# Performance work log

Measured on AMD Instinct MI355X. Metric: run time of the kernel, lower is better.

The kernel has to match this reference:

```python
import jax, jax.numpy as jnp
import numpy as np

B, S, E, H = 4, 2048, 1024, 16
D = E // H

def setup_inputs() -> dict:
    key = jax.random.key(0)
    ks = jax.random.split(key, 8)
    sc = lambda fan_in: 1.0 / np.sqrt(fan_in)
    return {
        "query": jax.random.normal(ks[0], (B, S, E), jnp.float32),
        "Wq": jax.random.normal(ks[1], (E, E), jnp.float32) * sc(E),
        "bq": jnp.zeros((E,), jnp.float32),
        "Wk": jax.random.normal(ks[2], (E, E), jnp.float32) * sc(E),
        "bk": jnp.zeros((E,), jnp.float32),
        "Wv": jax.random.normal(ks[3], (E, E), jnp.float32) * sc(E),
        "bv": jnp.zeros((E,), jnp.float32),
        "Wo": jax.random.normal(ks[4], (E, E), jnp.float32) * sc(E),
        "bo": jnp.zeros((E,), jnp.float32),
        "Wm1": jax.random.normal(ks[5], (E // 4, E), jnp.float32) * sc(E),
        "bm1": jnp.zeros((E // 4,), jnp.float32),
        "Wm2": jax.random.normal(ks[6], (E, E // 4), jnp.float32) * sc(E // 4),
        "bm2": jnp.zeros((E,), jnp.float32),
        "dopamine": jnp.ones((1,), jnp.float32),
        "serotonin": jnp.ones((1,), jnp.float32),
        "norepinephrine": jnp.ones((1,), jnp.float32),
        "acetylcholine": jnp.ones((1,), jnp.float32),
        "attn_scale": jnp.ones((1,), jnp.float32),
        "attn_bias": jnp.zeros((1,), jnp.float32),
    }

def reference(query, Wq, bq, Wk, bk, Wv, bv, Wo, bo,
              Wm1, bm1, Wm2, bm2,
              dopamine, serotonin, norepinephrine, acetylcholine,
              attn_scale, attn_bias):
    scale = D ** (-0.5)
    # projections (nn.Linear: y = x @ W.T + b)
    q = (query @ Wq.T + bq).reshape(B, S, H, D).transpose(0, 2, 1, 3)  # [B,H,S,D]
    k = (query @ Wk.T + bk).reshape(B, S, H, D).transpose(0, 2, 1, 3)
    v = (query @ Wv.T + bv).reshape(B, S, H, D).transpose(0, 2, 1, 3)
    scores = jnp.einsum('bhqd,bhkd->bhqk', q, k) * scale  # [B,H,S,S]
    probs = jax.nn.softmax(scores, axis=-1)
    attn = jnp.einsum('bhqk,bhkd->bhqd', probs, v)  # [B,H,S,D]
    # neuromodulation: MLP on query, summed scalar-weighted effects / 4
    mod = jax.nn.relu(query @ Wm1.T + bm1) @ Wm2.T + bm2  # [B,S,E]
    nm_gain = (dopamine + serotonin + norepinephrine + acetylcholine) / 4.0  # [1]
    neuromod = (mod * nm_gain).reshape(B, S, H, D).transpose(0, 2, 1, 3)  # [B,H,S,D]
    attn = (attn * attn_scale + attn_bias) * (1.0 + neuromod)
    attn = attn.transpose(0, 2, 1, 3).reshape(B, S, E)
    return attn @ Wo.T + bo
```

## Files before the change

kernel.cpp:

```cpp
#include <hip/hip_runtime.h>
#include <hip/hip_bf16.h>
#include <cstdint>

#define PB 4
#define PS 2048
#define PE 1024
#define PH 16
#define PD 64
#define PM (PB * PS)

typedef __attribute__((ext_vector_type(8))) _Float16 half8;
typedef __attribute__((ext_vector_type(4))) float f32x4;

#define MFMAH __builtin_amdgcn_mfma_f32_16x16x32_f16

#define GLOAD_LDS(gp, lp) __builtin_amdgcn_global_load_lds(                    \
    (const __attribute__((address_space(1))) void*)(gp),                       \
    (__attribute__((address_space(3))) void*)(lp), 16, 0, 0)

#if __has_builtin(__builtin_amdgcn_exp2f)
#define FAST_EXP2 1
#else
#define FAST_EXP2 0
#endif

__device__ inline unsigned short h16(float x) {
    _Float16 h = (_Float16)x;
    unsigned short u;
    __builtin_memcpy(&u, &h, 2);
    return u;
}
__device__ inline unsigned pkrtz(float a, float b) {
    auto p = __builtin_amdgcn_cvt_pkrtz(a, b);
    unsigned u;
    __builtin_memcpy(&u, &p, 4);
    return u;
}

__global__ __launch_bounds__(256)
void split_all(const float* __restrict__ q,   const float* __restrict__ wq,
               const float* __restrict__ wk,  const float* __restrict__ wv,
               const float* __restrict__ wo,  const float* __restrict__ wm1,
               const float* __restrict__ wm2,
               unsigned short* qh,  unsigned short* wqh, unsigned short* wkh,
               unsigned short* wvh, unsigned short* woh,
               unsigned short* m1h, unsigned short* m2h)
{
    const int b = blockIdx.x;
    const float* src; unsigned short* dst; int base;
    if      (b <  8192) { src = q;   dst = qh;  base = 0;     }
    else if (b <  9216) { src = wq;  dst = wqh; base = 8192;  }
    else if (b < 10240) { src = wk;  dst = wkh; base = 9216;  }
    else if (b < 11264) { src = wv;  dst = wvh; base = 10240; }
    else if (b < 12288) { src = wo;  dst = woh; base = 11264; }
    else if (b < 12544) { src = wm1; dst = m1h; base = 12288; }
    else                { src = wm2; dst = m2h; base = 12544; }
    const int i = (b - base) * 256 + threadIdx.x;
    float4 f = ((const float4*)src)[i];
    ushort4 h;
    h.x = h16(f.x); h.y = h16(f.y); h.z = h16(f.z); h.w = h16(f.w);
    ((ushort4*)dst)[i] = h;
}

template<int MODE, bool RELU>
__global__ __launch_bounds__(256, 2)
void gemm_pl(const unsigned short* __restrict__ Ah,
             const unsigned short* __restrict__ Bh,
             const float* __restrict__ bias, float* __restrict__ C,
             unsigned short* __restrict__ Oh,
             int M, int N, int K,
             const float* __restrict__ attn,
             const float* __restrict__ g0, const float* __restrict__ g1,
             const float* __restrict__ g2, const float* __restrict__ g3,
             const float* __restrict__ asc, const float* __restrict__ abi)
{
    __shared__ int4 ldsq[4096];
    char* const lds = (char*)ldsq;

    const int tid  = threadIdx.x;
    const int lane = tid & 63;
    const int w    = tid >> 6;
    const int lq   = lane & 15;
    const int lg   = lane >> 4;
    const int wm   = (w >> 1) * 64;
    const int wn   = (w & 1) * 64;
    const int m0   = blockIdx.x * 128;
    const int n0   = blockIdx.y * 128;

    const unsigned short* const gp =
        (w < 2) ? Ah + (size_t)m0 * K : Bh + (size_t)n0 * K;
    const int pb    = (w < 2) ? 0 : 16384;
    const int ch0   = (w & 1) * 8;
    const int scol8 = (((lane & 7) ^ (lane >> 3)) << 3);
    const int lrow8 = lane >> 3;

    auto ISSUE = [&](int k0, int bufn) {
        #pragma unroll
        for (int r = 0; r < 8; ++r) {
            const int c   = ch0 + r;
            const int row = c * 8 + lrow8;
            GLOAD_LDS(gp + (size_t)row * K + k0 + scol8,
                      lds + bufn * 32768 + pb + c * 1024 + 16 * lane);
        }
    };

    f32x4 acc[4][4];
    #pragma unroll
    for (int mt = 0; mt < 4; ++mt)
        #pragma unroll
        for (int nt = 0; nt < 4; ++nt)
            acc[mt][nt] = (f32x4){0.f, 0.f, 0.f, 0.f};

    ISSUE(0, 0);
    __syncthreads();

    int buf = 0;
    for (int k0 = 0; k0 < K; k0 += 64) {
        if (k0 + 64 < K) ISSUE(k0 + 64, buf ^ 1);

        const char* const L = lds + buf * 32768;
        #pragma unroll
        for (int kh = 0; kh < 2; ++kh) {
            half8 af[4];
            #pragma unroll
            for (int mt = 0; mt < 4; ++mt) {
                const int row = wm + 16 * mt + lq;
                const int off = row * 128 + ((kh * 64 + 16 * lg) ^ ((row & 7) << 4));
                af[mt] = *(const half8*)(L + off);
            }
            #pragma unroll
            for (int nt = 0; nt < 4; ++nt) {
                const int row = wn + 16 * nt + lq;
                const int off = row * 128 + ((kh * 64 + 16 * lg) ^ ((row & 7) << 4));
                half8 bf = *(const half8*)(L + 16384 + off);
                #pragma unroll
                for (int mt = 0; mt < 4; ++mt)
                    acc[mt][nt] = MFMAH(af[mt], bf, acc[mt][nt], 0, 0, 0);
            }
        }
        __syncthreads();
        buf ^= 1;
    }

    float gain = 0.f, ascv = 0.f, abiv = 0.f;
    if (MODE == 6) {
        gain = 0.25f * (*g0 + *g1 + *g2 + *g3);
        ascv = *asc;
        abiv = *abi;
    }

    #pragma unroll
    for (int nt = 0; nt < 4; ++nt) {
        const int n  = n0 + wn + 16 * nt + lq;
        const float bv = bias[n];
        #pragma unroll
        for (int mt = 0; mt < 4; ++mt) {
            #pragma unroll
            for (int j = 0; j < 4; ++j) {
                const int m = m0 + wm + 16 * mt + 4 * lg + j;
                float v = acc[mt][nt][j] + bv;
                if (RELU) v = fmaxf(v, 0.f);
                if (MODE == 0) {
                    C[(size_t)m * N + n] = v;
                } else if (MODE == 1) {
                    const int b = m >> 11, s = m & 2047;
                    const int h = n >> 6, d = n & 63;
                    C[((size_t)(b * PH + h) * PS + s) * PD + d] = v;
                } else if (MODE == 3) {
                    const int b = m >> 11, s = m & 2047;
                    const int h = n >> 6, d = n & 63;
                    Oh[((size_t)(b * PH + h) * PS + s) * PD + d] = h16(v);
                } else if (MODE == 4) {
                    const int b = m >> 11;
                    const int h = n >> 6, d = n & 63;
                    const int scol = (m & 2047 & ~63) + ((mt & 1) << 5)
                                   + (lg << 3) + ((mt >> 1) << 2) + j;
                    Oh[((size_t)(b * PH + h) * PD + d) * PS + scol] = h16(v);
                } else if (MODE == 5) {
                    Oh[(size_t)m * N + n] = h16(v);
                } else {
                    const int b = m >> 11, s = m & 2047;
                    const int h = n >> 6, d = n & 63;
                    const float av = attn[((size_t)(b * PH + h) * PS + s) * PD + d];
                    const float o = (av * ascv + abiv) * (1.f + v * gain);
                    Oh[(size_t)m * N + n] = h16(o);
                }
            }
        }
    }
}

typedef __attribute__((ext_vector_type(8))) short short8;
#define MFMA16 __builtin_amdgcn_mfma_f32_16x16x32_bf16
__device__ inline unsigned short bf16rn(float x) {
    unsigned u = __builtin_bit_cast(unsigned, x);
    u += 0x7FFFu + ((u >> 16) & 1u);
    return (unsigned short)(u >> 16);
}
__device__ inline float bf16tof(unsigned short h) {
    unsigned u = ((unsigned)h) << 16;
    return __builtin_bit_cast(float, u);
}
__device__ inline void split2(float x, unsigned short& h, unsigned short& l) {
    h = bf16rn(x);
    l = bf16rn(x - bf16tof(h));
}

template<int MODE, bool RELU>
__global__ __launch_bounds__(256, 2)
void gemm_nt(const float* __restrict__ A, const float* __restrict__ Bw,
             const float* __restrict__ bias, float* __restrict__ C,
             unsigned short* __restrict__ Ohi,
             int M, int N, int K,
             const float* __restrict__ attn,
             const float* __restrict__ g0, const float* __restrict__ g1,
             const float* __restrict__ g2, const float* __restrict__ g3,
             const float* __restrict__ asc, const float* __restrict__ abi)
{
    __shared__ int4 ldsq[4096];
    char* const lds = (char*)ldsq;

    const int tid  = threadIdx.x;
    const int lane = tid & 63;
    const int w    = tid >> 6;
    const int lq   = lane & 15;
    const int lg   = lane >> 4;
    const int wm   = (w >> 1) * 64;
    const int wn   = (w & 1) * 64;
    const int m0   = blockIdx.x * 128;
    const int n0   = blockIdx.y * 128;

    const int irow = tid >> 3;
    const int ic8  = (tid & 7) * 8;
    const int woff = (ic8 * 2);

    f32x4 acc[4][4];
    #pragma unroll
    for (int mt = 0; mt < 4; ++mt)
        #pragma unroll
        for (int nt = 0; nt < 4; ++nt)
            acc[mt][nt] = (f32x4){0.f, 0.f, 0.f, 0.f};

    for (int k0 = 0; k0 < K; k0 += 64) {
        #pragma unroll
        for (int mat = 0; mat < 2; ++mat) {
            const float* const src = mat ? Bw : A;
            const int rbase = mat ? n0 : m0;
            const int pbase = mat ? 32768 : 0;
            #pragma unroll
            for (int r = 0; r < 4; ++r) {
                const int row = irow + 32 * r;
                const float* p = src + (size_t)(rbase + row) * K + k0 + ic8;
                float4 f0 = *(const float4*)p;
                float4 f1 = *(const float4*)(p + 4);
                short8 vh, vl;
                {
                    unsigned short h, l;
                    split2(f0.x, h, l); vh[0] = (short)h; vl[0] = (short)l;
                    split2(f0.y, h, l); vh[1] = (short)h; vl[1] = (short)l;
                    split2(f0.z, h, l); vh[2] = (short)h; vl[2] = (short)l;
                    split2(f0.w, h, l); vh[3] = (short)h; vl[3] = (short)l;
                    split2(f1.x, h, l); vh[4] = (short)h; vl[4] = (short)l;
                    split2(f1.y, h, l); vh[5] = (short)h; vl[5] = (short)l;
                    split2(f1.z, h, l); vh[6] = (short)h; vl[6] = (short)l;
                    split2(f1.w, h, l); vh[7] = (short)h; vl[7] = (short)l;
                }
                const int off = row * 128 + (woff ^ ((row & 7) << 4));
                *(short8*)(lds + pbase + off)         = vh;
                *(short8*)(lds + pbase + 16384 + off) = vl;
            }
        }
        __syncthreads();

        #pragma unroll
        for (int kh = 0; kh < 2; ++kh) {
            short8 afh[4], afl[4];
            #pragma unroll
            for (int mt = 0; mt < 4; ++mt) {
                const int row = wm + 16 * mt + lq;
                const int off = row * 128 + ((kh * 64 + 16 * lg) ^ ((row & 7) << 4));
                afh[mt] = *(const short8*)(lds + off);
                afl[mt] = *(const short8*)(lds + 16384 + off);
            }
            #pragma unroll
            for (int nt = 0; nt < 4; ++nt) {
                const int row = wn + 16 * nt + lq;
                const int off = row * 128 + ((kh * 64 + 16 * lg) ^ ((row & 7) << 4));
                short8 bfh = *(const short8*)(lds + 32768 + off);
                short8 bfl = *(const short8*)(lds + 49152 + off);
                #pragma unroll
                for (int mt = 0; mt < 4; ++mt) {
                    acc[mt][nt] = MFMA16(afh[mt], bfh, acc[mt][nt], 0, 0, 0);
                    acc[mt][nt] = MFMA16(afh[mt], bfl, acc[mt][nt], 0, 0, 0);
                    acc[mt][nt] = MFMA16(afl[mt], bfh, acc[mt][nt], 0, 0, 0);
                }
            }
        }
        __syncthreads();
    }

    float gain = 0.f, ascv = 0.f, abiv = 0.f;
    if (MODE == 2) {
        gain = 0.25f * (*g0 + *g1 + *g2 + *g3);
        ascv = *asc;
        abiv = *abi;
    }

    #pragma unroll
    for (int nt = 0; nt < 4; ++nt) {
        const int n  = n0 + wn + 16 * nt + lq;
        const float bv = bias[n];
        #pragma unroll
        for (int mt = 0; mt < 4; ++mt) {
            #pragma unroll
            for (int j = 0; j < 4; ++j) {
                const int m = m0 + wm + 16 * mt + 4 * lg + j;
                float v = acc[mt][nt][j] + bv;
                if (RELU) v = fmaxf(v, 0.f);
                if (MODE == 0) {
                    C[(size_t)m * N + n] = v;
                } else if (MODE == 1) {
                    const int b = m >> 11, s = m & 2047;
                    const int h = n >> 6, d = n & 63;
                    C[((size_t)(b * PH + h) * PS + s) * PD + d] = v;
                } else if (MODE == 3) {
                    const int b = m >> 11, s = m & 2047;
                    const int h = n >> 6, d = n & 63;
                    Ohi[((size_t)(b * PH + h) * PS + s) * PD + d] = h16(v);
                } else if (MODE == 4) {
                    const int b = m >> 11;
                    const int h = n >> 6, d = n & 63;
                    const int scol = (m & 2047 & ~63) + ((mt & 1) << 5)
                                   + (lg << 3) + ((mt >> 1) << 2) + j;
                    Ohi[((size_t)(b * PH + h) * PD + d) * PS + scol] = h16(v);
                } else {
                    const int b = m >> 11, s = m & 2047;
                    const int h = n >> 6, d = n & 63;
                    const float av = attn[((size_t)(b * PH + h) * PS + s) * PD + d];
                    C[(size_t)m * N + n] = (av * ascv + abiv) * (1.f + v * gain);
                }
            }
        }
    }
}

__global__ __launch_bounds__(256, 2)
void flash_mfma(const float* qf,
                const unsigned short* __restrict__ kf,
                const unsigned short* __restrict__ vtf,
                float* attn)
{
    __shared__ int4 ldsv[2048];
    char* const ldsb = (char*)ldsv;

    const int tid  = threadIdx.x;
    const int lane = tid & 63;
    const int w    = tid >> 6;
    const int lq   = lane & 15;
    const int lg   = lane >> 4;

    const int L  = blockIdx.x + (blockIdx.y << 4) + (blockIdx.z << 8);
    const int nL = ((L & 7) << 7) + (L >> 3);
    const int bh = nL >> 4;
    const int q0 = (nL & 15) * 128 + w * 32;

    const size_t kbase = (size_t)bh * PS * PD;
    const size_t vbase = (size_t)bh * PD * PS;

    const unsigned short* const gp = (w < 2) ? kf + kbase : vtf + vbase;
    const bool isK = (w < 2);
    const int ch0   = (w & 1) * 4;
    const int scol8 = (((lane & 7) ^ (lane >> 3)) << 3);
    const int lrow8 = lane >> 3;

    auto ISSUE = [&](int kt, int bufn) {
        #pragma unroll
        for (int r = 0; r < 4; ++r) {
            const int c   = ch0 + r;
            const int row = c * 8 + lrow8;
            const size_t goff = isK ? (size_t)(kt + row) * PD + scol8
                                    : (size_t)row * PS + kt + scol8;
            GLOAD_LDS(gp + goff,
                      ldsb + bufn * 16384 + (isK ? 0 : 8192) + c * 1024 + 16 * lane);
        }
    };

    const half8 onesh = {(_Float16)1.f, (_Float16)1.f, (_Float16)1.f,
                         (_Float16)1.f, (_Float16)1.f, (_Float16)1.f,
                         (_Float16)1.f, (_Float16)1.f};

#if FAST_EXP2
    const float QSCALE = 0.125f * 1.4426950408889634f;
    const float THR    = 11.5415603f;
#define EXP_P(x) __builtin_amdgcn_exp2f(x)
#else
    const float QSCALE = 0.125f;
    const float THR    = 8.f;
#define EXP_P(x) __expf(x)
#endif

    half8 qh[2][2];
    #pragma unroll
    for (int u = 0; u < 2; ++u) {
        const float* qp = qf + ((size_t)bh * PS + q0 + 16 * u + lq) * PD + 8 * lg;
        #pragma unroll
        for (int t = 0; t < 2; ++t)
            #pragma unroll
            for (int b = 0; b < 8; ++b)
                qh[u][t][b] = (_Float16)(qp[t * 32 + b] * QSCALE);
    }

    f32x4 ot[2][4];
    #pragma unroll
    for (int u = 0; u < 2; ++u)
        #pragma unroll
        for (int mt = 0; mt < 4; ++mt)
            ot[u][mt] = (f32x4){0.f, 0.f, 0.f, 0.f};
    f32x4 lacc[2] = {{0.f,0.f,0.f,0.f}, {0.f,0.f,0.f,0.f}};
    float m_run[2] = {-3.0e38f, -3.0e38f};

    ISSUE(0, 0);
    __syncthreads();

    int buf = 0;
    for (int kti = 0; kti < PS / 64; ++kti) {
        const bool pf = (kti + 1 < PS / 64);
        if (pf) ISSUE((kti + 1) * 64, buf ^ 1);

        const char* const L2 = ldsb + buf * 16384;

        f32x4 st[2][4];
        #pragma unroll
        for (int mt = 0; mt < 4; ++mt) {
            const int row = 16 * mt + lq;
            const int swz = (row & 7) << 4;
            const char* kr = L2 + row * 128;
            half8 a0 = *(const half8*)(kr + ((16 * lg) ^ swz));
            half8 a1 = *(const half8*)(kr + ((64 + 16 * lg) ^ swz));
            #pragma unroll
            for (int u = 0; u < 2; ++u) {
                f32x4 acc = {0.f, 0.f, 0.f, 0.f};
                acc = MFMAH(a0, qh[u][0], acc, 0, 0, 0);
                acc = MFMAH(a1, qh[u][1], acc, 0, 0, 0);
                st[u][mt] = acc;
            }
        }

        half8 pb[2][2];
        #pragma unroll
        for (int u = 0; u < 2; ++u) {
            float a0 = fmaxf(fmaxf(st[u][0][0], st[u][0][1]), st[u][0][2]);
            float a1 = fmaxf(fmaxf(st[u][0][3], st[u][1][0]), st[u][1][1]);
            float a2 = fmaxf(fmaxf(st[u][1][2], st[u][1][3]), st[u][2][0]);
            float a3 = fmaxf(fmaxf(st[u][2][1], st[u][2][2]), st[u][2][3]);
            float a4 = fmaxf(fmaxf(st[u][3][0], st[u][3][1]), st[u][3][2]);
            float b0 = fmaxf(fmaxf(a0, a1), a2);
            float b1 = fmaxf(fmaxf(a3, a4), st[u][3][3]);
            float pmax = fmaxf(b0, b1);
            pmax = fmaxf(pmax, __shfl_xor(pmax, 16));
            pmax = fmaxf(pmax, __shfl_xor(pmax, 32));
            if (!__all(pmax - m_run[u] <= THR)) {
                float mnew = fmaxf(m_run[u], pmax);
                float corr = EXP_P(m_run[u] - mnew);
                m_run[u] = mnew;
                #pragma unroll
                for (int j = 0; j < 4; ++j)
                    lacc[u][j] *= corr;
                #pragma unroll
                for (int mt = 0; mt < 4; ++mt)
                    #pragma unroll
                    for (int j = 0; j < 4; ++j)
                        ot[u][mt][j] *= corr;
            }
            #pragma unroll
            for (int mt = 0; mt < 4; ++mt)
                #pragma unroll
                for (int j = 0; j < 4; ++j)
                    st[u][mt][j] = EXP_P(st[u][mt][j] - m_run[u]);
            #pragma unroll
            for (int t = 0; t < 2; ++t) {
                unsigned w0 = pkrtz(st[u][t][0],     st[u][t][1]);
                unsigned w1 = pkrtz(st[u][t][2],     st[u][t][3]);
                unsigned w2 = pkrtz(st[u][t + 2][0], st[u][t + 2][1]);
                unsigned w3 = pkrtz(st[u][t + 2][2], st[u][t + 2][3]);
                uint4 pw = make_uint4(w0, w1, w2, w3);
                __builtin_memcpy(&pb[u][t], &pw, 16);
            }
            lacc[u] = MFMAH(onesh, pb[u][0], lacc[u], 0, 0, 0);
            lacc[u] = MFMAH(onesh, pb[u][1], lacc[u], 0, 0, 0);
        }

        #pragma unroll
        for (int t = 0; t < 2; ++t) {
            #pragma unroll
            for (int mt = 0; mt < 4; ++mt) {
                const int row = 16 * mt + lq;
                const int swz = (row & 7) << 4;
                const char* vr = L2 + 8192 + row * 128;
                half8 vv = *(const half8*)(vr + ((t * 64 + 16 * lg) ^ swz));
                #pragma unroll
                for (int u = 0; u < 2; ++u)
                    ot[u][mt] = MFMAH(vv, pb[u][t], ot[u][mt], 0, 0, 0);
            }
        }

        __syncthreads();
        buf ^= 1;
    }

    #pragma unroll
    for (int u = 0; u < 2; ++u) {
        const float inv = 1.f / lacc[u][0];
        float* op = attn + ((size_t)bh * PS + q0 + 16 * u + lq) * PD + 4 * lg;
        #pragma unroll
        for (int mt = 0; mt < 4; ++mt) {
            float4 o;
            o.x = ot[u][mt][0] * inv; o.y = ot[u][mt][1] * inv;
            o.z = ot[u][mt][2] * inv; o.w = ot[u][mt][3] * inv;
            *(float4*)(op + 16 * mt) = o;
        }
    }
}

extern "C" void kernel_launch(void* const* d_in, const int* in_sizes, int n_in,
                              void* d_out, int out_size, void* d_ws, size_t ws_size,
                              hipStream_t stream)
{
    const float* query = (const float*)d_in[0];
    const float* Wq  = (const float*)d_in[1];  const float* bq  = (const float*)d_in[2];
    const float* Wk  = (const float*)d_in[3];  const float* bk  = (const float*)d_in[4];
    const float* Wv  = (const float*)d_in[5];  const float* bv  = (const float*)d_in[6];
    const float* Wo  = (const float*)d_in[7];  const float* bo  = (const float*)d_in[8];
    const float* Wm1 = (const float*)d_in[9];  const float* bm1 = (const float*)d_in[10];
    const float* Wm2 = (const float*)d_in[11]; const float* bm2 = (const float*)d_in[12];
    const float* dop = (const float*)d_in[13];
    const float* ser = (const float*)d_in[14];
    const float* nor = (const float*)d_in[15];
    const float* ach = (const float*)d_in[16];
    const float* asc = (const float*)d_in[17];
    const float* abi = (const float*)d_in[18];
    float* out = (float*)d_out;

    char* wsb = (char*)d_ws;
    float*          qf32 = (float*)wsb;
    unsigned short* kf   = (unsigned short*)(wsb + (32u << 20));
    unsigned short* vtf  = (unsigned short*)(wsb + (48u << 20));

    dim3 blk(256);
    const bool presplit = (ws_size >= 161480704ull);

    if (presplit) {
        unsigned short* h1h   = (unsigned short*)(wsb + (64u << 20));
        unsigned short* afh   = (unsigned short*)(wsb + (72u << 20));
        unsigned short* qh    = (unsigned short*)(wsb + (104u << 20));
        unsigned short* wqh   = (unsigned short*)(wsb + (136u << 20));
        unsigned short* wkh   = (unsigned short*)(wsb + (138u << 20));
        unsigned short* wvh   = (unsigned short*)(wsb + (140u << 20));
        unsigned short* woh   = (unsigned short*)(wsb + (142u << 20));
        unsigned short* m1h   = (unsigned short*)(wsb + (144u << 20));
        unsigned short* m2h   = (unsigned short*)(wsb + (145u << 20));

        split_all<<<12800, blk, 0, stream>>>(
            query, Wq, Wk, Wv, Wo, Wm1, Wm2,
            qh, wqh, wkh, wvh, woh, m1h, m2h);

        gemm_pl<1, false><<<dim3(PM / 128, PE / 128), blk, 0, stream>>>(
            qh, wqh, bq, qf32, nullptr, PM, PE, PE,
            nullptr, nullptr, nullptr, nullptr, nullptr, nullptr, nullptr);
        gemm_pl<3, false><<<dim3(PM / 128, PE / 128), blk, 0, stream>>>(
            qh, wkh, bk, nullptr, kf, PM, PE, PE,
            nullptr, nullptr, nullptr, nullptr, nullptr, nullptr, nullptr);
        gemm_pl<4, false><<<dim3(PM / 128, PE / 128), blk, 0, stream>>>(
            qh, wvh, bv, nullptr, vtf, PM, PE, PE,
            nullptr, nullptr, nullptr, nullptr, nullptr, nullptr, nullptr);
        gemm_pl<5, true><<<dim3(PM / 128, 256 / 128), blk, 0, stream>>>(
            qh, m1h, bm1, nullptr, h1h, PM, 256, PE,
            nullptr, nullptr, nullptr, nullptr, nullptr, nullptr, nullptr);

        flash_mfma<<<dim3(PS / 128, PH, PB), blk, 0, stream>>>(
            qf32, kf, vtf, qf32);

        gemm_pl<6, false><<<dim3(PM / 128, PE / 128), blk, 0, stream>>>(
            h1h, m2h, bm2, nullptr, afh, PM, PE, 256,
            qf32, dop, ser, nor, ach, asc, abi);
        gemm_pl<0, false><<<dim3(PM / 128, PE / 128), blk, 0, stream>>>(
            afh, woh, bo, out, nullptr, PM, PE, PE,
            nullptr, nullptr, nullptr, nullptr, nullptr, nullptr, nullptr);
    } else {
        float* h1    = (float*)(wsb + (64u << 20));
        float* attnf = (float*)(wsb + (72u << 20));

        gemm_nt<1, false><<<dim3(PM / 128, PE / 128), blk, 0, stream>>>(
            query, Wq, bq, qf32, nullptr, PM, PE, PE,
            nullptr, nullptr, nullptr, nullptr, nullptr, nullptr, nullptr);
        gemm_nt<3, false><<<dim3(PM / 128, PE / 128), blk, 0, stream>>>(
            query, Wk, bk, nullptr, kf, PM, PE, PE,
            nullptr, nullptr, nullptr, nullptr, nullptr, nullptr, nullptr);
        gemm_nt<4, false><<<dim3(PM / 128, PE / 128), blk, 0, stream>>>(
            query, Wv, bv, nullptr, vtf, PM, PE, PE,
            nullptr, nullptr, nullptr, nullptr, nullptr, nullptr, nullptr);
        gemm_nt<0, true><<<dim3(PM / 128, 256 / 128), blk, 0, stream>>>(
            query, Wm1, bm1, h1, nullptr, PM, 256, PE,
            nullptr, nullptr, nullptr, nullptr, nullptr, nullptr, nullptr);

        flash_mfma<<<dim3(PS / 128, PH, PB), blk, 0, stream>>>(
            qf32, kf, vtf, qf32);

        gemm_nt<2, false><<<dim3(PM / 128, PE / 128), blk, 0, stream>>>(
            h1, Wm2, bm2, attnf, nullptr, PM, PE, 256,
            qf32, dop, ser, nor, ach, asc, abi);
        gemm_nt<0, false><<<dim3(PM / 128, PE / 128), blk, 0, stream>>>(
            attnf, Wo, bo, out, nullptr, PM, PE, PE,
            nullptr, nullptr, nullptr, nullptr, nullptr, nullptr, nullptr);
    }
}
```

Measured before the change: 228.4 us.

## Fuse Q, K, V projections into one GEMM kernel sharing the A tile

Replaces three separate projection GEMM launches with a single 512-thread kernel that loads one 128-row activation tile and three 128-column weight tiles per K step. Each block computes Q, K and V outputs together, so the shared input tile is read from global memory once instead of three times and two launches go away. The cost is 128 KB of double-buffered LDS per block and a larger accumulator footprint per thread, which can limit occupancy.

```diff
diff --git a/kernel.cpp b/kernel.cpp
--- a/kernel.cpp
+++ b/kernel.cpp
@@ -62,6 +62,118 @@
     ((ushort4*)dst)[i] = h;
 }
 
+__global__ __launch_bounds__(512, 2)
+void gemm_qkv(const unsigned short* __restrict__ Ah,
+              const unsigned short* __restrict__ Wqh,
+              const unsigned short* __restrict__ Wkh,
+              const unsigned short* __restrict__ Wvh,
+              const float* __restrict__ bq, const float* __restrict__ bk,
+              const float* __restrict__ bv,
+              float* __restrict__ qf32, unsigned short* __restrict__ kf,
+              unsigned short* __restrict__ vtf)
+{
+    __shared__ int4 ldsq[8192];
+    char* const lds = (char*)ldsq;
+    const int K = PE;
+
+    const int tid  = threadIdx.x;
+    const int lane = tid & 63;
+    const int w    = tid >> 6;
+    const int lq   = lane & 15;
+    const int lg   = lane >> 4;
+    const int wr   = w >> 2;
+    const int wc   = w & 3;
+    const int m0   = blockIdx.x * 128;
+    const int n0   = blockIdx.y * 128;
+
+    const int plane = w >> 1;
+    const unsigned short* const gp =
+        (plane == 0) ? Ah  + (size_t)m0 * K :
+        (plane == 1) ? Wqh + (size_t)n0 * K :
+        (plane == 2) ? Wkh + (size_t)n0 * K :
+                       Wvh + (size_t)n0 * K;
+    const int pbase = plane * 16384;
+    const int ch0   = (w & 1) * 8;
+    const int scol8 = (((lane & 7) ^ (lane >> 3)) << 3);
+    const int lrow8 = lane >> 3;
+
+    auto ISSUE = [&](int k0, int bufn) {
+        #pragma unroll
+        for (int r = 0; r < 8; ++r) {
+            const int c   = ch0 + r;
+            const int row = c * 8 + lrow8;
+            GLOAD_LDS(gp + (size_t)row * K + k0 + scol8,
+                      lds + bufn * 65536 + pbase + c * 1024 + 16 * lane);
+        }
+    };
+
+    f32x4 acc[3][4][2];
+    #pragma unroll
+    for (int o = 0; o < 3; ++o)
+        #pragma unroll
+        for (int mt = 0; mt < 4; ++mt)
+            #pragma unroll
+            for (int nt = 0; nt < 2; ++nt)
+                acc[o][mt][nt] = (f32x4){0.f, 0.f, 0.f, 0.f};
+
+    ISSUE(0, 0);
+    __syncthreads();
+
+    int buf = 0;
+    for (int k0 = 0; k0 < K; k0 += 64) {
+        if (k0 + 64 < K) ISSUE(k0 + 64, buf ^ 1);
+
+        const char* const L = lds + buf * 65536;
+        #pragma unroll
+        for (int kh = 0; kh < 2; ++kh) {
+            half8 af[4];
+            #pragma unroll
+            for (int mt = 0; mt < 4; ++mt) {
+                const int row = 64 * wr + 16 * mt + lq;
+                const int off = row * 128 + ((kh * 64 + 16 * lg) ^ ((row & 7) << 4));
+                af[mt] = *(const half8*)(L + off);
+            }
+            #pragma unroll
+            for (int o = 0; o < 3; ++o) {
+                #pragma unroll
+                for (int nt = 0; nt < 2; ++nt) {
+                    const int row = 32 * wc + 16 * nt + lq;
+                    const int off = row * 128 + ((kh * 64 + 16 * lg) ^ ((row & 7) << 4));
+                    half8 bf = *(const half8*)(L + 16384 * (o + 1) + off);
+                    #pragma unroll
+                    for (int mt = 0; mt < 4; ++mt)
+                        acc[o][mt][nt] = MFMAH(af[mt], bf, acc[o][mt][nt], 0, 0, 0);
+                }
+            }
+        }
+        __syncthreads();
+        buf ^= 1;
+    }
+
+    #pragma unroll
+    for (int nt = 0; nt < 2; ++nt) {
+        const int n = n0 + 32 * wc + 16 * nt + lq;
+        const int h = n >> 6, d = n & 63;
+        const float bqv = bq[n], bkv = bk[n], bvv = bv[n];
+        #pragma unroll
+        for (int mt = 0; mt < 4; ++mt) {
+            #pragma unroll
+            for (int j = 0; j < 4; ++j) {
+                const int m = m0 + 64 * wr + 16 * mt + 4 * lg + j;
+                const int b = m >> 11, s = m & 2047;
+                qf32[((size_t)(b * PH + h) * PS + s) * PD + d] =
+                    acc[0][mt][nt][j] + bqv;
+                kf[((size_t)(b * PH + h) * PS + s) * PD + d] =
+                    h16(acc[1][mt][nt][j] + bkv);
+                const int scol = (s & ~63) + ((mt & 1) << 5) + (lg << 3)
+                               + ((mt >> 1) << 2) + j;
+                vtf[((size_t)(b * PH + h) * PD + d) * PS + scol] =
+                    h16(acc[2][mt][nt][j] + bvv);
+            }
+        }
+    }
+}
+
 template<int MODE, bool RELU>
 __global__ __launch_bounds__(256, 2)
 void gemm_pl(const unsigned short* __restrict__ Ah,
@@ -162,20 +274,6 @@
                 if (RELU) v = fmaxf(v, 0.f);
                 if (MODE == 0) {
                     C[(size_t)m * N + n] = v;
-                } else if (MODE == 1) {
-                    const int b = m >> 11, s = m & 2047;
-                    const int h = n >> 6, d = n & 63;
-                    C[((size_t)(b * PH + h) * PS + s) * PD + d] = v;
-                } else if (MODE == 3) {
-                    const int b = m >> 11, s = m & 2047;
-                    const int h = n >> 6, d = n & 63;
-                    Oh[((size_t)(b * PH + h) * PS + s) * PD + d] = h16(v);
-                } else if (MODE == 4) {
-                    const int b = m >> 11;
-                    const int h = n >> 6, d = n & 63;
-                    const int scol = (m & 2047 & ~63) + ((mt & 1) << 5)
-                                   + (lg << 3) + ((mt >> 1) << 2) + j;
-                    Oh[((size_t)(b * PH + h) * PD + d) * PS + scol] = h16(v);
                 } else if (MODE == 5) {
                     Oh[(size_t)m * N + n] = h16(v);
                 } else {
@@ -564,15 +662,9 @@
             query, Wq, Wk, Wv, Wo, Wm1, Wm2,
             qh, wqh, wkh, wvh, woh, m1h, m2h);
 
-        gemm_pl<1, false><<<dim3(PM / 128, PE / 128), blk, 0, stream>>>(
-            qh, wqh, bq, qf32, nullptr, PM, PE, PE,
-            nullptr, nullptr, nullptr, nullptr, nullptr, nullptr, nullptr);
-        gemm_pl<3, false><<<dim3(PM / 128, PE / 128), blk, 0, stream>>>(
-            qh, wkh, bk, nullptr, kf, PM, PE, PE,
-            nullptr, nullptr, nullptr, nullptr, nullptr, nullptr, nullptr);
-        gemm_pl<4, false><<<dim3(PM / 128, PE / 128), blk, 0, stream>>>(
-            qh, wvh, bv, nullptr, vtf, PM, PE, PE,
-            nullptr, nullptr, nullptr, nullptr, nullptr, nullptr, nullptr);
+        gemm_qkv<<<dim3(PM / 128, PE / 128), dim3(512), 0, stream>>>(
+            qh, wqh, wkh, wvh, bq, bk, bv, qf32, kf, vtf);
+
         gemm_pl<5, true><<<dim3(PM / 128, 256 / 128), blk, 0, stream>>>(
             qh, m1h, bm1, nullptr, h1h, PM, 256, PE,
             nullptr, nullptr, nullptr, nullptr, nullptr, nullptr, nullptr);
```

After: 223.4 us. -2.2%, faster.
